# Performance work log

Hardware: AMD Instinct MI355X
Metric: run time of the kernel (lower is better)

Reference implementation:

```python
import jax, jax.numpy as jnp
import numpy as np

# Natural-order 4x4 Hadamard matrix (H @ H = 4*I); 2D inverse WHT scale = 1/16.
H4 = np.array([[1, 1, 1, 1],
               [1, -1, 1, -1],
               [1, 1, -1, -1],
               [1, -1, -1, 1]], dtype=np.float32)

B, NH, NW, C, K = 16, 28, 28, 64, 64  # out_channels=192 -> K=64 per branch


def setup_inputs() -> dict:
    key = jax.random.key(0)
    ks = jax.random.split(key, 9)
    d = {}
    for i, n in enumerate(['transIm1', 'transIm2', 'transIm3']):
        d[n] = jax.random.normal(ks[i], (16, B, NH, NW, C), dtype=jnp.float32)
    for i, n in enumerate(['weight1', 'weight2', 'weight3']):
        d[n] = jax.random.normal(ks[3 + i], (16, C, K), dtype=jnp.float32) * 0.05
    for i, n in enumerate(['bias1', 'bias2', 'bias3']):
        d[n] = jax.random.normal(ks[6 + i], (1, 1, 1, K), dtype=jnp.float32) * 0.05
    return d


def _iwht_branch(trans, w, b):
    # Per-WHT-coefficient channel matmul: [16,B,nH,nW,C] x [16,C,K] -> [16,B,nH,nW,K]
    y = jnp.einsum('tbijc,tck->tbijk', trans, w)
    _, Bb, nH, nW, Kk = y.shape
    y = y.reshape(4, 4, Bb, nH, nW, Kk)  # coeff index t = 4*u + v
    h = jnp.asarray(H4, y.dtype)
    # Inverse 2D WHT per 4x4 block, scatter blocks back to pixel grid.
    z = jnp.einsum('pu,qv,uvbijk->bipjqk', h, h, y) * (1.0 / 16.0)
    return z.reshape(Bb, 4 * nH, 4 * nW, Kk) + b


def reference(transIm1, transIm2, transIm3, weight1, weight2, weight3,
              bias1, bias2, bias3):
    out1 = _iwht_branch(transIm1, weight1, bias1)
    out2 = _iwht_branch(transIm2, weight2, bias2)
    out3 = _iwht_branch(transIm3, weight3, bias3)
    return (out1, out2, out3)
```

## Files before the change

kernel.cpp:

```cpp
#include <hip/hip_runtime.h>
#include <hip/hip_bf16.h>


typedef __attribute__((ext_vector_type(8))) short bf16x8;
typedef __attribute__((ext_vector_type(4))) float floatx4;
typedef __attribute__((ext_vector_type(4))) float f32x4;

#define NSITES 12544
#define NTILES 784
#define OUT_PER_BRANCH 12845056
#define WT_ELEMS (3*16*64*64)

__device__ __forceinline__ short f32_to_bf16_bits(float f) {
    __hip_bfloat16 h = __float2bfloat16(f);
    return *reinterpret_cast<short*>(&h);
}

__global__ void transpose_weights(const float* __restrict__ w0,
                                  const float* __restrict__ w1,
                                  const float* __restrict__ w2,
                                  __hip_bfloat16* __restrict__ wT) {
    int idx = blockIdx.x * blockDim.x + threadIdx.x;
    if (idx >= WT_ELEMS) return;
    int c  = idx & 63;
    int k  = (idx >> 6) & 63;
    int t  = (idx >> 12) & 15;
    int br = idx >> 16;
    const float* w = (br == 0) ? w0 : ((br == 1) ? w1 : w2);
    wT[idx] = __float2bfloat16(w[(t * 64 + c) * 64 + k]);
}

template <bool USE_WT>
__global__ __launch_bounds__(256) void iwht_kernel(
    const float* __restrict__ x0, const float* __restrict__ x1,
    const float* __restrict__ x2,
    const float* __restrict__ w0, const float* __restrict__ w1,
    const float* __restrict__ w2,
    const __hip_bfloat16* __restrict__ wT,
    const float* __restrict__ b0, const float* __restrict__ b1,
    const float* __restrict__ b2,
    float* __restrict__ out) {
    int bx   = blockIdx.x;
    int br   = bx / NTILES;
    int tile = bx - br * NTILES;
    int lane = threadIdx.x & 63;
    int wave = threadIdx.x >> 6;
    int l15  = lane & 15;
    int quad = lane >> 4;
    int n    = wave * 16 + l15;

    const float* x    = (br == 0) ? x0 : ((br == 1) ? x1 : x2);
    const float* w    = (br == 0) ? w0 : ((br == 1) ? w1 : w2);
    const float* bias = (br == 0) ? b0 : ((br == 1) ? b1 : b2);

    int srow = tile * 16 + l15;

    floatx4 acc[16];
#pragma unroll
    for (int t = 0; t < 16; t++) acc[t] = (floatx4){0.f, 0.f, 0.f, 0.f};

    const float* xbase = x + (size_t)srow * 64 + quad * 8;

#pragma unroll
    for (int t = 0; t < 16; t++) {
        const f32x4* xv = reinterpret_cast<const f32x4*>(xbase + (size_t)t * NSITES * 64);
        f32x4 f0 = xv[0], f1 = xv[1];
        f32x4 f2 = xv[8], f3 = xv[9];
        bf16x8 a0, a1;
#pragma unroll
        for (int j = 0; j < 4; j++) {
            a0[j]     = f32_to_bf16_bits(f0[j]);
            a0[j + 4] = f32_to_bf16_bits(f1[j]);
            a1[j]     = f32_to_bf16_bits(f2[j]);
            a1[j + 4] = f32_to_bf16_bits(f3[j]);
        }
        bf16x8 bb0, bb1;
        if (USE_WT) {
            const bf16x8* wv = reinterpret_cast<const bf16x8*>(
                wT + (((size_t)(br * 16 + t) * 64 + n) * 64) + quad * 8);
            bb0 = wv[0];
            bb1 = wv[4];
        } else {
#pragma unroll
            for (int j = 0; j < 8; j++) {
                int c0 = quad * 8 + j;
                bb0[j] = f32_to_bf16_bits(w[(t * 64 + c0) * 64 + n]);
                bb1[j] = f32_to_bf16_bits(w[(t * 64 + c0 + 32) * 64 + n]);
            }
        }
        acc[t] = __builtin_amdgcn_mfma_f32_16x16x32_bf16(a0, bb0, acc[t], 0, 0, 0);
        acc[t] = __builtin_amdgcn_mfma_f32_16x16x32_bf16(a1, bb1, acc[t], 0, 0, 0);
    }

    float biasf = bias[n];

    size_t obase[4];
#pragma unroll
    for (int r = 0; r < 4; r++) {
        int site = tile * 16 + quad * 4 + r;
        int b    = site / 784;
        int rem  = site - b * 784;
        int i    = rem / 28;
        int j    = rem - i * 28;
        obase[r] = (size_t)br * OUT_PER_BRANCH +
                   (((size_t)(b * 112 + 4 * i)) * 112 + 4 * j) * 64 + n;
    }

#pragma unroll
    for (int u = 0; u < 4; u++) {
        floatx4 y0 = acc[4 * u + 0], y1 = acc[4 * u + 1];
        floatx4 y2 = acc[4 * u + 2], y3 = acc[4 * u + 3];
        floatx4 A = y0 + y2, Bv = y1 + y3, Cv = y0 - y2, Dv = y1 - y3;
        acc[4 * u + 0] = A + Bv;
        acc[4 * u + 1] = A - Bv;
        acc[4 * u + 2] = Cv + Dv;
        acc[4 * u + 3] = Cv - Dv;
    }

#pragma unroll
    for (int q = 0; q < 4; q++) {
        floatx4 z0 = acc[0 + q], z1 = acc[4 + q], z2 = acc[8 + q], z3 = acc[12 + q];
        floatx4 A = z0 + z2, Bv = z1 + z3, Cv = z0 - z2, Dv = z1 - z3;
        floatx4 o[4];
        o[0] = A + Bv;
        o[1] = A - Bv;
        o[2] = Cv + Dv;
        o[3] = Cv - Dv;
#pragma unroll
        for (int p = 0; p < 4; p++) {
#pragma unroll
            for (int r = 0; r < 4; r++) {
                float v = o[p][r] * 0.0625f + biasf;
                out[obase[r] + (size_t)(p * 112 + q) * 64] = v;
            }
        }
    }
}

extern "C" void kernel_launch(void* const* d_in, const int* in_sizes, int n_in,
                              void* d_out, int out_size, void* d_ws, size_t ws_size,
                              hipStream_t stream) {
    const float* x0 = (const float*)d_in[0];
    const float* x1 = (const float*)d_in[1];
    const float* x2 = (const float*)d_in[2];
    const float* w0 = (const float*)d_in[3];
    const float* w1 = (const float*)d_in[4];
    const float* w2 = (const float*)d_in[5];
    const float* b0 = (const float*)d_in[6];
    const float* b1 = (const float*)d_in[7];
    const float* b2 = (const float*)d_in[8];
    float* out = (float*)d_out;
    __hip_bfloat16* wT = (__hip_bfloat16*)d_ws;

    bool use_wt = ws_size >= (size_t)WT_ELEMS * sizeof(__hip_bfloat16);
    if (use_wt) {
        transpose_weights<<<(WT_ELEMS + 255) / 256, 256, 0, stream>>>(w0, w1, w2, wT);
        iwht_kernel<true><<<3 * NTILES, 256, 0, stream>>>(x0, x1, x2, w0, w1, w2, wT,
                                                          b0, b1, b2, out);
    } else {
        iwht_kernel<false><<<3 * NTILES, 256, 0, stream>>>(x0, x1, x2, w0, w1, w2, wT,
                                                           b0, b1, b2, out);
    }
}
```

Before: 340.5 us.

## Stage input tiles in LDS with double-buffered async global-to-LDS loads

Replaces the per-wave direct global reads of the activation rows with a block-wide staging step into shared memory. It uses global_load_lds, four coefficient slices per stage, and double buffering across four stages. Before, all four waves read the same 16 sites from global memory. Now each row is fetched once per block and the waves read it from padded LDS rows. The cost is 34 KB of LDS per block, which lowers occupancy, plus extra barriers. Correctness relies on the async LDS loads being complete at each barrier.

```diff
diff --git a/kernel.cpp b/kernel.cpp
--- a/kernel.cpp
+++ b/kernel.cpp
@@ -4,12 +4,13 @@
 
 typedef __attribute__((ext_vector_type(8))) short bf16x8;
 typedef __attribute__((ext_vector_type(4))) float floatx4;
-typedef __attribute__((ext_vector_type(4))) float f32x4;
 
 #define NSITES 12544
 #define NTILES 784
 #define OUT_PER_BRANCH 12845056
 #define WT_ELEMS (3*16*64*64)
+#define ROW_F 68
+#define CHUNK_F (64 * ROW_F)
 
 __device__ __forceinline__ short f32_to_bf16_bits(float f) {
     __hip_bfloat16 h = __float2bfloat16(f);
@@ -40,6 +41,8 @@
     const float* __restrict__ b0, const float* __restrict__ b1,
     const float* __restrict__ b2,
     float* __restrict__ out) {
+    __shared__ float xs[2][CHUNK_F];
+
     int bx   = blockIdx.x;
     int br   = bx / NTILES;
     int tile = bx - br * NTILES;
@@ -53,44 +56,69 @@
     const float* w    = (br == 0) ? w0 : ((br == 1) ? w1 : w2);
     const float* bias = (br == 0) ? b0 : ((br == 1) ? b1 : b2);
 
-    int srow = tile * 16 + l15;
+    const float* xg = x + (size_t)(tile * 16) * 64 + lane;
 
     floatx4 acc[16];
 #pragma unroll
     for (int t = 0; t < 16; t++) acc[t] = (floatx4){0.f, 0.f, 0.f, 0.f};
 
-    const float* xbase = x + (size_t)srow * 64 + quad * 8;
+#define STAGE(g, buf)                                                          \
+    {                                                                          \
+        _Pragma("unroll") for (int r = 0; r < 16; r++) {                       \
+            int row = wave * 16 + r;                      \
+            int tl  = row >> 4;                                                \
+            int s   = row & 15;                                                \
+            const float* gp = xg + ((size_t)((g) * 4 + tl) * NSITES + s) * 64; \
+            __builtin_amdgcn_global_load_lds(                                  \
+                (const __attribute__((address_space(1))) void*)gp,             \
+                (__attribute__((address_space(3))) void*)&xs[buf][row * ROW_F],\
+                4, 0, 0);                                                      \
+        }                                                                      \
+    }
+
+    STAGE(0, 0);
+    __syncthreads();
 
 #pragma unroll
-    for (int t = 0; t < 16; t++) {
-        const f32x4* xv = reinterpret_cast<const f32x4*>(xbase + (size_t)t * NSITES * 64);
-        f32x4 f0 = xv[0], f1 = xv[1];
-        f32x4 f2 = xv[8], f3 = xv[9];
-        bf16x8 a0, a1;
+    for (int g = 0; g < 4; g++) {
+        int buf = g & 1;
+        if (g < 3) STAGE(g + 1, buf ^ 1);
 #pragma unroll
-        for (int j = 0; j < 4; j++) {
-            a0[j]     = f32_to_bf16_bits(f0[j]);
-            a0[j + 4] = f32_to_bf16_bits(f1[j]);
-            a1[j]     = f32_to_bf16_bits(f2[j]);
-            a1[j + 4] = f32_to_bf16_bits(f3[j]);
+        for (int tl = 0; tl < 4; tl++) {
+            int t = g * 4 + tl;
+            const float* rowp = &xs[buf][(tl * 16 + l15) * ROW_F + quad * 8];
+            floatx4 f0 = ((const floatx4*)rowp)[0];
+            floatx4 f1 = ((const floatx4*)rowp)[1];
+            floatx4 f2 = ((const floatx4*)(rowp + 32))[0];
+            floatx4 f3 = ((const floatx4*)(rowp + 32))[1];
+            bf16x8 a0, a1;
+#pragma unroll
+            for (int j = 0; j < 4; j++) {
+                a0[j]     = f32_to_bf16_bits(f0[j]);
+                a0[j + 4] = f32_to_bf16_bits(f1[j]);
+                a1[j]     = f32_to_bf16_bits(f2[j]);
+                a1[j + 4] = f32_to_bf16_bits(f3[j]);
+            }
+            bf16x8 bb0, bb1;
+            if (USE_WT) {
+                const bf16x8* wv = reinterpret_cast<const bf16x8*>(
+                    wT + (((size_t)(br * 16 + t) * 64 + n) * 64) + quad * 8);
+                bb0 = wv[0];
+                bb1 = wv[4];
+            } else {
+#pragma unroll
+                for (int j = 0; j < 8; j++) {
+                    int c0 = quad * 8 + j;
+                    bb0[j] = f32_to_bf16_bits(w[(t * 64 + c0) * 64 + n]);
+                    bb1[j] = f32_to_bf16_bits(w[(t * 64 + c0 + 32) * 64 + n]);
+                }
+            }
+            acc[t] = __builtin_amdgcn_mfma_f32_16x16x32_bf16(a0, bb0, acc[t], 0, 0, 0);
+            acc[t] = __builtin_amdgcn_mfma_f32_16x16x32_bf16(a1, bb1, acc[t], 0, 0, 0);
         }
-        bf16x8 bb0, bb1;
-        if (USE_WT) {
-            const bf16x8* wv = reinterpret_cast<const bf16x8*>(
-                wT + (((size_t)(br * 16 + t) * 64 + n) * 64) + quad * 8);
-            bb0 = wv[0];
-            bb1 = wv[4];
-        } else {
-#pragma unroll
-            for (int j = 0; j < 8; j++) {
-                int c0 = quad * 8 + j;
-                bb0[j] = f32_to_bf16_bits(w[(t * 64 + c0) * 64 + n]);
-                bb1[j] = f32_to_bf16_bits(w[(t * 64 + c0 + 32) * 64 + n]);
-            }
-        }
-        acc[t] = __builtin_amdgcn_mfma_f32_16x16x32_bf16(a0, bb0, acc[t], 0, 0, 0);
-        acc[t] = __builtin_amdgcn_mfma_f32_16x16x32_bf16(a1, bb1, acc[t], 0, 0, 0);
+        if (g < 3) __syncthreads();
     }
+#undef STAGE
 
     float biasf = bias[n];
 
```

New measurement: 301.1 us. -11.6%, faster.
